# Performance work log

Measured on AMD Instinct MI355X. Metric: run time of the kernel, lower is better.

## Reference

```python
import jax, jax.numpy as jnp
import numpy as np

N = 10000       # n_nodes
E = 640000      # n_edges (avg degree 64)
D_IN = 128      # in_feats
D_H = 128       # n_hidden
N_CLS = 64      # n_classes


def setup_inputs() -> dict:
    key = jax.random.key(0)
    k1, k2, k3, k4, k5, k6 = jax.random.split(key, 6)
    features = jax.random.normal(k1, (N, D_IN), dtype=jnp.float32)
    src = jax.random.randint(k2, (E,), 0, N, dtype=jnp.int32)
    dst = jax.random.randint(k3, (E,), 0, N, dtype=jnp.int32)
    s = 0.05  # small init scale to keep activations bounded across 3 layers
    # Stored as [in, out]; equivalent to torch Linear weight [out, in] transposed.
    W0 = jax.random.normal(k4, (D_IN, D_H), dtype=jnp.float32) * s
    W1 = jax.random.normal(k5, (D_H, D_H), dtype=jnp.float32) * s
    W2 = jax.random.normal(k6, (D_H, N_CLS), dtype=jnp.float32) * s
    return {"features": features, "W0": W0, "W1": W1, "W2": W2,
            "src": src, "dst": dst}


def reference(features, W0, W1, W2, src, dst):
    # GINConv with aggregator 'sum', eps=0 (learn_eps=False):
    #   h' = Linear(h + sum_{(u->v) in E} h[u] scattered to v)
    # Dropout is identity at inference; 'activation' is unused in the module.
    def gin_layer(h, W):
        agg = jax.ops.segment_sum(h[src], dst, num_segments=N)  # [N, d]
        return (h + agg) @ W

    h = gin_layer(features, W0)
    h = gin_layer(h, W1)
    h = gin_layer(h, W2)
    return h
```

## Files before the change

kernel.cpp:

```cpp
#include <hip/hip_runtime.h>
#include <hip/hip_bf16.h>

#define NN 10000
#define NE 640000
#define D_IN 128
#define D_H 128
#define N_CLS 64
#define CAP 160
#define GRP 157
#define CAPC 4800
#define CCS 16
#define SENT 10000
#define EPB 1024
#define AB 625
#define CB 1251
#define WB 80

__device__ __forceinline__ float blo(unsigned u) { return __uint_as_float(u << 16); }
__device__ __forceinline__ float bhi(unsigned u) { return __uint_as_float(u & 0xffff0000u); }
__device__ __forceinline__ unsigned short f2bf(float f) {
    unsigned u = __float_as_uint(f);
    return (unsigned short)((u + 0x7fffu + ((u >> 16) & 1u)) >> 16);
}
__device__ __forceinline__ unsigned packbf(float a, float b) {
    return (unsigned)f2bf(a) | ((unsigned)f2bf(b) << 16);
}

__global__ __launch_bounds__(256) void prep_a(const int* __restrict__ src,
                                              const int* __restrict__ dst,
                                              int* __restrict__ coarse_cnt,
                                              unsigned* __restrict__ coarse,
                                              const float* __restrict__ feat,
                                              unsigned* __restrict__ hb0,
                                              const float* __restrict__ W0,
                                              const float* __restrict__ W1,
                                              const float* __restrict__ W2,
                                              unsigned* __restrict__ wb0,
                                              unsigned* __restrict__ wb1,
                                              unsigned* __restrict__ wb2) {
    int bid = blockIdx.x;
    if (bid >= AB + CB) {
        int t = (bid - AB - CB) * 256 + threadIdx.x;
        if (t < 8192) {
            int kp = t >> 7, j = t & 127;
            wb0[t] = packbf(W0[(2 * kp) * 128 + j], W0[(2 * kp + 1) * 128 + j]);
        } else if (t < 16384) {
            int tt = t - 8192, kp = tt >> 7, j = tt & 127;
            wb1[tt] = packbf(W1[(2 * kp) * 128 + j], W1[(2 * kp + 1) * 128 + j]);
        } else if (t < 20480) {
            int tt = t - 16384, kp = tt >> 6, j = tt & 63;
            wb2[tt] = packbf(W2[(2 * kp) * 64 + j], W2[(2 * kp + 1) * 64 + j]);
        }
        return;
    }
    if (bid >= AB) {
        int t = (bid - AB) * 256 + threadIdx.x;
        if (t < NN * 32) {
            float4 f = ((const float4*)feat)[t];
            ((uint2*)hb0)[t] = make_uint2(packbf(f.x, f.y), packbf(f.z, f.w));
        } else if (t < (NN + 1) * 32) {
            ((uint2*)hb0)[t] = make_uint2(0u, 0u);
        }
        return;
    }
    __shared__ unsigned stage[EPB];
    __shared__ int hist[GRP], gbase[GRP], cur[GRP];
    const int t = threadIdx.x;
    for (int i = t; i < GRP; i += 256) hist[i] = 0;
    __syncthreads();
    const int e0 = bid * EPB;
    for (int i = t; i < EPB; i += 256) {
        int s = src[e0 + i];
        int d = dst[e0 + i];
        stage[i] = (unsigned)s | ((unsigned)d << 16);
        atomicAdd(&hist[d >> 6], 1);
    }
    __syncthreads();
    for (int i = t; i < GRP; i += 256) {
        gbase[i] = atomicAdd(&coarse_cnt[i * CCS], hist[i]);
        cur[i] = 0;
    }
    __syncthreads();
    for (int i = t; i < EPB; i += 256) {
        unsigned u = stage[i];
        int g = u >> 22;
        int r = atomicAdd(&cur[g], 1);
        coarse[g * CAPC + gbase[g] + r] = u;
    }
}

__global__ __launch_bounds__(1024) void prep_b(const int* __restrict__ coarse_cnt,
                                               const unsigned* __restrict__ coarse,
                                               int* __restrict__ cnt,
                                               unsigned short* __restrict__ colbuf) {
    __shared__ int cur[64];
    __shared__ unsigned short sbuf[64][CAP];
    const int g = blockIdx.x;
    const int t = threadIdx.x;
    if (t < 64) cur[t] = 0;
    __syncthreads();
    const int m = coarse_cnt[g * CCS];
    const unsigned* cb = coarse + g * CAPC;
    for (int i = t; i < m; i += 1024) {
        unsigned u = cb[i];
        int s = (int)(u & 0xFFFFu);
        int dl = (int)(u >> 16) - (g << 6);
        int r = atomicAdd(&cur[dl], 1);
        sbuf[dl][r] = (unsigned short)s;
    }
    __syncthreads();
    if (t < 64) {
        int n = (g << 6) + t;
        if (n < NN) {
            int c = cur[t];
            int pad = (32 - (c & 31)) & 31;
            for (int k = 0; k < pad; ++k) sbuf[t][c + k] = (unsigned short)SENT;
            cnt[n] = c + pad;
        }
    }
    __syncthreads();
    const uint4* s4 = (const uint4*)sbuf;
    for (int idx = t; idx < 64 * (CAP / 8); idx += 1024) {
        int node = (g << 6) + (idx / (CAP / 8));
        if (node < NN)
            ((uint4*)colbuf)[(size_t)node * (CAP / 8) + (idx % (CAP / 8))] = s4[idx];
    }
}

__global__ __launch_bounds__(256, 4) void gin_layer1(const uint4* __restrict__ hb4,
                                                     const int* __restrict__ cnt,
                                                     const unsigned short* __restrict__ colbuf,
                                                     const unsigned* __restrict__ Wb,
                                                     unsigned short* __restrict__ outb) {
    constexpr int M = 4;
    __shared__ float xs[M][D_H];
    const int base = blockIdx.x * M;
    const int tid = threadIdx.x;
    const int wave = tid >> 6;
    const int lane = tid & 63;
    const int sub = lane >> 4;
    const int off = lane & 15;

    const int n = __builtin_amdgcn_readfirstlane(base + wave);
    float a0, a1, a2, a3, a4, a5, a6, a7;
    if (sub == 0) {
        uint4 u = hb4[n * 16 + off];
        a0 = blo(u.x); a1 = bhi(u.x); a2 = blo(u.y); a3 = bhi(u.y);
        a4 = blo(u.z); a5 = bhi(u.z); a6 = blo(u.w); a7 = bhi(u.w);
    } else {
        a0 = a1 = a2 = a3 = a4 = a5 = a6 = a7 = 0.f;
    }
    const int NCH = __builtin_amdgcn_readfirstlane(cnt[n]) >> 5;
    const uint2* cl = (const uint2*)(colbuf + n * CAP);
    const int sh = (sub & 1) << 4;
    uint2 p0 = cl[0], p1 = cl[1], p2 = cl[2], p3 = cl[3];
    uint2 p4 = cl[4], p5 = cl[5], p6 = cl[6], p7 = cl[7];
    for (int c = 0; c < NCH; ++c) {
        unsigned w0 = (sub & 2) ? p0.y : p0.x;
        unsigned w1 = (sub & 2) ? p1.y : p1.x;
        unsigned w2 = (sub & 2) ? p2.y : p2.x;
        unsigned w3 = (sub & 2) ? p3.y : p3.x;
        unsigned w4 = (sub & 2) ? p4.y : p4.x;
        unsigned w5 = (sub & 2) ? p5.y : p5.x;
        unsigned w6 = (sub & 2) ? p6.y : p6.x;
        unsigned w7 = (sub & 2) ? p7.y : p7.x;
        int s0 = (int)((w0 >> sh) & 0xffffu);
        int s1 = (int)((w1 >> sh) & 0xffffu);
        int s2 = (int)((w2 >> sh) & 0xffffu);
        int s3 = (int)((w3 >> sh) & 0xffffu);
        int s4 = (int)((w4 >> sh) & 0xffffu);
        int s5 = (int)((w5 >> sh) & 0xffffu);
        int s6 = (int)((w6 >> sh) & 0xffffu);
        int s7 = (int)((w7 >> sh) & 0xffffu);
        uint4 u0 = hb4[s0 * 16 + off];
        uint4 u1 = hb4[s1 * 16 + off];
        uint4 u2 = hb4[s2 * 16 + off];
        uint4 u3 = hb4[s3 * 16 + off];
        uint4 u4 = hb4[s4 * 16 + off];
        uint4 u5 = hb4[s5 * 16 + off];
        uint4 u6 = hb4[s6 * 16 + off];
        uint4 u7 = hb4[s7 * 16 + off];
        {
            const uint2* nx = cl + 8 * (c + 1);
            p0 = nx[0]; p1 = nx[1]; p2 = nx[2]; p3 = nx[3];
            p4 = nx[4]; p5 = nx[5]; p6 = nx[6]; p7 = nx[7];
        }
        a0 += ((blo(u0.x) + blo(u1.x)) + (blo(u2.x) + blo(u3.x)))
            + ((blo(u4.x) + blo(u5.x)) + (blo(u6.x) + blo(u7.x)));
        a1 += ((bhi(u0.x) + bhi(u1.x)) + (bhi(u2.x) + bhi(u3.x)))
            + ((bhi(u4.x) + bhi(u5.x)) + (bhi(u6.x) + bhi(u7.x)));
        a2 += ((blo(u0.y) + blo(u1.y)) + (blo(u2.y) + blo(u3.y)))
            + ((blo(u4.y) + blo(u5.y)) + (blo(u6.y) + blo(u7.y)));
        a3 += ((bhi(u0.y) + bhi(u1.y)) + (bhi(u2.y) + bhi(u3.y)))
            + ((bhi(u4.y) + bhi(u5.y)) + (bhi(u6.y) + bhi(u7.y)));
        a4 += ((blo(u0.z) + blo(u1.z)) + (blo(u2.z) + blo(u3.z)))
            + ((blo(u4.z) + blo(u5.z)) + (blo(u6.z) + blo(u7.z)));
        a5 += ((bhi(u0.z) + bhi(u1.z)) + (bhi(u2.z) + bhi(u3.z)))
            + ((bhi(u4.z) + bhi(u5.z)) + (bhi(u6.z) + bhi(u7.z)));
        a6 += ((blo(u0.w) + blo(u1.w)) + (blo(u2.w) + blo(u3.w)))
            + ((blo(u4.w) + blo(u5.w)) + (blo(u6.w) + blo(u7.w)));
        a7 += ((bhi(u0.w) + bhi(u1.w)) + (bhi(u2.w) + bhi(u3.w)))
            + ((bhi(u4.w) + bhi(u5.w)) + (bhi(u6.w) + bhi(u7.w)));
    }
    a0 += __shfl_xor(a0, 16); a0 += __shfl_xor(a0, 32);
    a1 += __shfl_xor(a1, 16); a1 += __shfl_xor(a1, 32);
    a2 += __shfl_xor(a2, 16); a2 += __shfl_xor(a2, 32);
    a3 += __shfl_xor(a3, 16); a3 += __shfl_xor(a3, 32);
    a4 += __shfl_xor(a4, 16); a4 += __shfl_xor(a4, 32);
    a5 += __shfl_xor(a5, 16); a5 += __shfl_xor(a5, 32);
    a6 += __shfl_xor(a6, 16); a6 += __shfl_xor(a6, 32);
    a7 += __shfl_xor(a7, 16); a7 += __shfl_xor(a7, 32);
    if (sub == 0) {
        *(float4*)&xs[wave][8 * off]     = make_float4(a0, a1, a2, a3);
        *(float4*)&xs[wave][8 * off + 4] = make_float4(a4, a5, a6, a7);
    }
    __syncthreads();

    constexpr int J = D_H;
    constexpr int G = 256 / J;
    constexpr int NM = M / G;
    const int gq = tid / J;
    const int j = tid % J;
    const int mbase = gq * NM;
    float acc[NM];
#pragma unroll
    for (int m = 0; m < NM; ++m) acc[m] = 0.f;
    for (int k = 0; k < D_H; k += 4) {
        unsigned wp0 = Wb[(k >> 1) * J + j];
        unsigned wp1 = Wb[((k >> 1) + 1) * J + j];
        float w0 = blo(wp0), w1 = bhi(wp0), w2 = blo(wp1), w3 = bhi(wp1);
#pragma unroll
        for (int m = 0; m < NM; ++m) {
            float4 xv = *(const float4*)&xs[mbase + m][k];
            acc[m] += xv.x * w0 + xv.y * w1 + xv.z * w2 + xv.w * w3;
        }
    }
#pragma unroll
    for (int m = 0; m < NM; ++m) {
        int n2 = base + mbase + m;
        outb[(size_t)n2 * J + j] = f2bf(acc[m]);
    }
    if (blockIdx.x == 0 && tid < 32) {
        ((uint2*)(outb + (size_t)SENT * D_H))[tid] = make_uint2(0u, 0u);
    }
}

__global__ __launch_bounds__(256, 4) void gin_mid(const uint4* __restrict__ hb4,
                                                  const int* __restrict__ cnt,
                                                  const unsigned short* __restrict__ colbuf,
                                                  const unsigned* __restrict__ Wb1,
                                                  const unsigned* __restrict__ Wb2,
                                                  unsigned short* __restrict__ tb) {
    constexpr int M = 4;
    __shared__ float xs[M][D_H];
    __shared__ float ys[M][136];
    const int base = blockIdx.x * M;
    const int tid = threadIdx.x;
    const int wave = tid >> 6;
    const int lane = tid & 63;
    const int sub = lane >> 4;
    const int off = lane & 15;

    const int n = __builtin_amdgcn_readfirstlane(base + wave);
    float a0, a1, a2, a3, a4, a5, a6, a7;
    if (sub == 0) {
        uint4 u = hb4[n * 16 + off];
        a0 = blo(u.x); a1 = bhi(u.x); a2 = blo(u.y); a3 = bhi(u.y);
        a4 = blo(u.z); a5 = bhi(u.z); a6 = blo(u.w); a7 = bhi(u.w);
    } else {
        a0 = a1 = a2 = a3 = a4 = a5 = a6 = a7 = 0.f;
    }
    const int NCH = __builtin_amdgcn_readfirstlane(cnt[n]) >> 5;
    const uint2* cl = (const uint2*)(colbuf + n * CAP);
    const int sh = (sub & 1) << 4;
    uint2 p0 = cl[0], p1 = cl[1], p2 = cl[2], p3 = cl[3];
    uint2 p4 = cl[4], p5 = cl[5], p6 = cl[6], p7 = cl[7];
    for (int c = 0; c < NCH; ++c) {
        unsigned w0 = (sub & 2) ? p0.y : p0.x;
        unsigned w1 = (sub & 2) ? p1.y : p1.x;
        unsigned w2 = (sub & 2) ? p2.y : p2.x;
        unsigned w3 = (sub & 2) ? p3.y : p3.x;
        unsigned w4 = (sub & 2) ? p4.y : p4.x;
        unsigned w5 = (sub & 2) ? p5.y : p5.x;
        unsigned w6 = (sub & 2) ? p6.y : p6.x;
        unsigned w7 = (sub & 2) ? p7.y : p7.x;
        int s0 = (int)((w0 >> sh) & 0xffffu);
        int s1 = (int)((w1 >> sh) & 0xffffu);
        int s2 = (int)((w2 >> sh) & 0xffffu);
        int s3 = (int)((w3 >> sh) & 0xffffu);
        int s4 = (int)((w4 >> sh) & 0xffffu);
        int s5 = (int)((w5 >> sh) & 0xffffu);
        int s6 = (int)((w6 >> sh) & 0xffffu);
        int s7 = (int)((w7 >> sh) & 0xffffu);
        uint4 u0 = hb4[s0 * 16 + off];
        uint4 u1 = hb4[s1 * 16 + off];
        uint4 u2 = hb4[s2 * 16 + off];
        uint4 u3 = hb4[s3 * 16 + off];
        uint4 u4 = hb4[s4 * 16 + off];
        uint4 u5 = hb4[s5 * 16 + off];
        uint4 u6 = hb4[s6 * 16 + off];
        uint4 u7 = hb4[s7 * 16 + off];
        {
            const uint2* nx = cl + 8 * (c + 1);
            p0 = nx[0]; p1 = nx[1]; p2 = nx[2]; p3 = nx[3];
            p4 = nx[4]; p5 = nx[5]; p6 = nx[6]; p7 = nx[7];
        }
        a0 += ((blo(u0.x) + blo(u1.x)) + (blo(u2.x) + blo(u3.x)))
            + ((blo(u4.x) + blo(u5.x)) + (blo(u6.x) + blo(u7.x)));
        a1 += ((bhi(u0.x) + bhi(u1.x)) + (bhi(u2.x) + bhi(u3.x)))
            + ((bhi(u4.x) + bhi(u5.x)) + (bhi(u6.x) + bhi(u7.x)));
        a2 += ((blo(u0.y) + blo(u1.y)) + (blo(u2.y) + blo(u3.y)))
            + ((blo(u4.y) + blo(u5.y)) + (blo(u6.y) + blo(u7.y)));
        a3 += ((bhi(u0.y) + bhi(u1.y)) + (bhi(u2.y) + bhi(u3.y)))
            + ((bhi(u4.y) + bhi(u5.y)) + (bhi(u6.y) + bhi(u7.y)));
        a4 += ((blo(u0.z) + blo(u1.z)) + (blo(u2.z) + blo(u3.z)))
            + ((blo(u4.z) + blo(u5.z)) + (blo(u6.z) + blo(u7.z)));
        a5 += ((bhi(u0.z) + bhi(u1.z)) + (bhi(u2.z) + bhi(u3.z)))
            + ((bhi(u4.z) + bhi(u5.z)) + (bhi(u6.z) + bhi(u7.z)));
        a6 += ((blo(u0.w) + blo(u1.w)) + (blo(u2.w) + blo(u3.w)))
            + ((blo(u4.w) + blo(u5.w)) + (blo(u6.w) + blo(u7.w)));
        a7 += ((bhi(u0.w) + bhi(u1.w)) + (bhi(u2.w) + bhi(u3.w)))
            + ((bhi(u4.w) + bhi(u5.w)) + (bhi(u6.w) + bhi(u7.w)));
    }
    a0 += __shfl_xor(a0, 16); a0 += __shfl_xor(a0, 32);
    a1 += __shfl_xor(a1, 16); a1 += __shfl_xor(a1, 32);
    a2 += __shfl_xor(a2, 16); a2 += __shfl_xor(a2, 32);
    a3 += __shfl_xor(a3, 16); a3 += __shfl_xor(a3, 32);
    a4 += __shfl_xor(a4, 16); a4 += __shfl_xor(a4, 32);
    a5 += __shfl_xor(a5, 16); a5 += __shfl_xor(a5, 32);
    a6 += __shfl_xor(a6, 16); a6 += __shfl_xor(a6, 32);
    a7 += __shfl_xor(a7, 16); a7 += __shfl_xor(a7, 32);
    if (sub == 0) {
        *(float4*)&xs[wave][8 * off]     = make_float4(a0, a1, a2, a3);
        *(float4*)&xs[wave][8 * off + 4] = make_float4(a4, a5, a6, a7);
    }
    __syncthreads();

    {
        constexpr int J = D_H;
        constexpr int G = 256 / J;
        constexpr int NM = M / G;
        const int gq = tid / J;
        const int j = tid % J;
        const int mbase = gq * NM;
        float acc[NM];
#pragma unroll
        for (int m = 0; m < NM; ++m) acc[m] = 0.f;
        for (int k = 0; k < D_H; k += 4) {
            unsigned wp0 = Wb1[(k >> 1) * J + j];
            unsigned wp1 = Wb1[((k >> 1) + 1) * J + j];
            float w0 = blo(wp0), w1 = bhi(wp0), w2 = blo(wp1), w3 = bhi(wp1);
#pragma unroll
            for (int m = 0; m < NM; ++m) {
                float4 xv = *(const float4*)&xs[mbase + m][k];
                acc[m] += xv.x * w0 + xv.y * w1 + xv.z * w2 + xv.w * w3;
            }
        }
#pragma unroll
        for (int m = 0; m < NM; ++m) ys[mbase + m][j] = acc[m];
    }
    __syncthreads();

    {
        constexpr int J = N_CLS;
        const int j = tid & 63;
        const int gm = tid >> 6;
        float acc = 0.f;
        for (int k = 0; k < D_H; k += 4) {
            unsigned wp0 = Wb2[(k >> 1) * J + j];
            unsigned wp1 = Wb2[((k >> 1) + 1) * J + j];
            float w0 = blo(wp0), w1 = bhi(wp0), w2 = blo(wp1), w3 = bhi(wp1);
            float4 xv = *(const float4*)&ys[gm][k];
            acc += xv.x * w0 + xv.y * w1 + xv.z * w2 + xv.w * w3;
        }
        tb[(size_t)(base + gm) * J + j] = f2bf(acc);
    }
    if (blockIdx.x == 0 && tid < 16) {
        ((uint2*)(tb + (size_t)SENT * N_CLS))[tid] = make_uint2(0u, 0u);
    }
}

__global__ __launch_bounds__(256, 4) void agg3(const uint4* __restrict__ tb4,
                                               const int* __restrict__ cnt,
                                               const unsigned short* __restrict__ colbuf,
                                               float* __restrict__ outf) {
    constexpr int M = 4;
    const int base = blockIdx.x * M;
    const int tid = threadIdx.x;
    const int wave = tid >> 6;
    const int lane = tid & 63;
    const int sub = lane >> 3;
    const int off = lane & 7;

    const int n = __builtin_amdgcn_readfirstlane(base + wave);
    float a0, a1, a2, a3, a4, a5, a6, a7;
    if (sub == 0) {
        uint4 u = tb4[n * 8 + off];
        a0 = blo(u.x); a1 = bhi(u.x); a2 = blo(u.y); a3 = bhi(u.y);
        a4 = blo(u.z); a5 = bhi(u.z); a6 = blo(u.w); a7 = bhi(u.w);
    } else {
        a0 = a1 = a2 = a3 = a4 = a5 = a6 = a7 = 0.f;
    }
    const int NCH = __builtin_amdgcn_readfirstlane(cnt[n]) >> 5;
    const uint2* cl = (const uint2*)(colbuf + n * CAP);
    const int hi4 = sub >> 2;
    const int wsel = (sub >> 1) & 1;
    const int sh = (sub & 1) << 4;
    uint2 p0 = cl[0], p1 = cl[1], p2 = cl[2], p3 = cl[3];
    uint2 p4 = cl[4], p5 = cl[5], p6 = cl[6], p7 = cl[7];
    for (int c = 0; c < NCH; ++c) {
        unsigned q0 = hi4 ? (wsel ? p1.y : p1.x) : (wsel ? p0.y : p0.x);
        unsigned q1 = hi4 ? (wsel ? p3.y : p3.x) : (wsel ? p2.y : p2.x);
        unsigned q2 = hi4 ? (wsel ? p5.y : p5.x) : (wsel ? p4.y : p4.x);
        unsigned q3 = hi4 ? (wsel ? p7.y : p7.x) : (wsel ? p6.y : p6.x);
        int s0 = (int)((q0 >> sh) & 0xffffu);
        int s1 = (int)((q1 >> sh) & 0xffffu);
        int s2 = (int)((q2 >> sh) & 0xffffu);
        int s3 = (int)((q3 >> sh) & 0xffffu);
        uint4 u0 = tb4[s0 * 8 + off];
        uint4 u1 = tb4[s1 * 8 + off];
        uint4 u2 = tb4[s2 * 8 + off];
        uint4 u3 = tb4[s3 * 8 + off];
        {
            const uint2* nx = cl + 8 * (c + 1);
            p0 = nx[0]; p1 = nx[1]; p2 = nx[2]; p3 = nx[3];
            p4 = nx[4]; p5 = nx[5]; p6 = nx[6]; p7 = nx[7];
        }
        a0 += (blo(u0.x) + blo(u1.x)) + (blo(u2.x) + blo(u3.x));
        a1 += (bhi(u0.x) + bhi(u1.x)) + (bhi(u2.x) + bhi(u3.x));
        a2 += (blo(u0.y) + blo(u1.y)) + (blo(u2.y) + blo(u3.y));
        a3 += (bhi(u0.y) + bhi(u1.y)) + (bhi(u2.y) + bhi(u3.y));
        a4 += (blo(u0.z) + blo(u1.z)) + (blo(u2.z) + blo(u3.z));
        a5 += (bhi(u0.z) + bhi(u1.z)) + (bhi(u2.z) + bhi(u3.z));
        a6 += (blo(u0.w) + blo(u1.w)) + (blo(u2.w) + blo(u3.w));
        a7 += (bhi(u0.w) + bhi(u1.w)) + (bhi(u2.w) + bhi(u3.w));
    }
    a0 += __shfl_xor(a0, 8); a0 += __shfl_xor(a0, 16); a0 += __shfl_xor(a0, 32);
    a1 += __shfl_xor(a1, 8); a1 += __shfl_xor(a1, 16); a1 += __shfl_xor(a1, 32);
    a2 += __shfl_xor(a2, 8); a2 += __shfl_xor(a2, 16); a2 += __shfl_xor(a2, 32);
    a3 += __shfl_xor(a3, 8); a3 += __shfl_xor(a3, 16); a3 += __shfl_xor(a3, 32);
    a4 += __shfl_xor(a4, 8); a4 += __shfl_xor(a4, 16); a4 += __shfl_xor(a4, 32);
    a5 += __shfl_xor(a5, 8); a5 += __shfl_xor(a5, 16); a5 += __shfl_xor(a5, 32);
    a6 += __shfl_xor(a6, 8); a6 += __shfl_xor(a6, 16); a6 += __shfl_xor(a6, 32);
    a7 += __shfl_xor(a7, 8); a7 += __shfl_xor(a7, 16); a7 += __shfl_xor(a7, 32);
    if (sub == 0) {
        float* o = outf + (size_t)n * N_CLS + 8 * off;
        *(float4*)o       = make_float4(a0, a1, a2, a3);
        *(float4*)(o + 4) = make_float4(a4, a5, a6, a7);
    }
}

extern "C" void kernel_launch(void* const* d_in, const int* in_sizes, int n_in,
                              void* d_out, int out_size, void* d_ws, size_t ws_size,
                              hipStream_t stream) {
    const float* feat = (const float*)d_in[0];
    const float* W0   = (const float*)d_in[1];
    const float* W1   = (const float*)d_in[2];
    const float* W2   = (const float*)d_in[3];
    const int*   src  = (const int*)d_in[4];
    const int*   dst  = (const int*)d_in[5];
    float* out = (float*)d_out;

    int* coarse_cnt        = (int*)d_ws;
    int* cnt               = coarse_cnt + GRP * CCS;
    unsigned short* colbuf = (unsigned short*)(cnt + NN + 8);
    unsigned* coarse       = (unsigned*)(colbuf + (size_t)NN * CAP);
    unsigned* hb0          = coarse + (size_t)GRP * CAPC;
    unsigned* hb1          = hb0 + (size_t)(NN + 1) * 64;
    unsigned* hb2          = hb1 + (size_t)(NN + 1) * 64;
    unsigned* wb0          = hb2 + (size_t)(NN + 1) * 64;
    unsigned* wb1          = wb0 + 8192;
    unsigned* wb2          = wb1 + 8192;
    unsigned short* tb     = (unsigned short*)hb2;

    hipMemsetAsync(coarse_cnt, 0, GRP * CCS * sizeof(int), stream);
    prep_a<<<AB + CB + WB, 256, 0, stream>>>(src, dst, coarse_cnt, coarse, feat, hb0,
                                             W0, W1, W2, wb0, wb1, wb2);
    prep_b<<<GRP, 1024, 0, stream>>>(coarse_cnt, coarse, cnt, colbuf);

    gin_layer1<<<NN / 4, 256, 0, stream>>>((const uint4*)hb0, cnt, colbuf, wb0,
                                           (unsigned short*)hb1);
    gin_mid<<<NN / 4, 256, 0, stream>>>((const uint4*)hb1, cnt, colbuf, wb1, wb2, tb);
    agg3<<<NN / 4, 256, 0, stream>>>((const uint4*)tb, cnt, colbuf, out);
}
```

Before: 142.9 us.

## Premultiply the three GIN weights and aggregate at 64-wide after one projection

Because the layers have no nonlinearity, the three weight matrices are multiplied together on device during prep (W0·W1, then ·W2, packed to bf16). The forward pass becomes one 128-wide aggregation with a single 128→64 projection, followed by two 64-wide aggregations. This removes the 128-wide middle gather and two per-node matmuls, cutting gather bandwidth. In exchange it adds small serial weight-product work in the prep kernels and changes bf16 rounding behaviour.

New measurement: 139.8 us. -2.2%, faster.

```diff
diff --git a/kernel.cpp b/kernel.cpp
--- a/kernel.cpp
+++ b/kernel.cpp
@@ -14,7 +14,8 @@
 #define EPB 1024
 #define AB 625
 #define CB 1251
-#define WB 80
+#define W01B 16
+#define WPB 4
 
 __device__ __forceinline__ float blo(unsigned u) { return __uint_as_float(u << 16); }
 __device__ __forceinline__ float bhi(unsigned u) { return __uint_as_float(u & 0xffff0000u); }
@@ -34,23 +35,19 @@
                                               unsigned* __restrict__ hb0,
                                               const float* __restrict__ W0,
                                               const float* __restrict__ W1,
-                                              const float* __restrict__ W2,
-                                              unsigned* __restrict__ wb0,
-                                              unsigned* __restrict__ wb1,
-                                              unsigned* __restrict__ wb2) {
+                                              float* __restrict__ W01) {
     int bid = blockIdx.x;
     if (bid >= AB + CB) {
         int t = (bid - AB - CB) * 256 + threadIdx.x;
-        if (t < 8192) {
-            int kp = t >> 7, j = t & 127;
-            wb0[t] = packbf(W0[(2 * kp) * 128 + j], W0[(2 * kp + 1) * 128 + j]);
-        } else if (t < 16384) {
-            int tt = t - 8192, kp = tt >> 7, j = tt & 127;
-            wb1[tt] = packbf(W1[(2 * kp) * 128 + j], W1[(2 * kp + 1) * 128 + j]);
-        } else if (t < 20480) {
-            int tt = t - 16384, kp = tt >> 6, j = tt & 63;
-            wb2[tt] = packbf(W2[(2 * kp) * 64 + j], W2[(2 * kp + 1) * 64 + j]);
-        }
+        int i = t >> 5;
+        int jb = (t & 31) << 2;
+        float c0 = 0.f, c1 = 0.f, c2 = 0.f, c3 = 0.f;
+        for (int k = 0; k < 128; ++k) {
+            float a = W0[i * 128 + k];
+            float4 b = *(const float4*)&W1[k * 128 + jb];
+            c0 += a * b.x; c1 += a * b.y; c2 += a * b.z; c3 += a * b.w;
+        }
+        *(float4*)&W01[i * 128 + jb] = make_float4(c0, c1, c2, c3);
         return;
     }
     if (bid >= AB) {
@@ -92,11 +89,28 @@
 __global__ __launch_bounds__(1024) void prep_b(const int* __restrict__ coarse_cnt,
                                                const unsigned* __restrict__ coarse,
                                                int* __restrict__ cnt,
-                                               unsigned short* __restrict__ colbuf) {
+                                               unsigned short* __restrict__ colbuf,
+                                               const float* __restrict__ W01,
+                                               const float* __restrict__ W2,
+                                               unsigned* __restrict__ wbp) {
+    const int g = blockIdx.x;
+    const int t = threadIdx.x;
+    if (g >= GRP) {
+        int s = (g - GRP) * 1024 + t;
+        int kp = s >> 6, j = s & 63;
+        float c0 = 0.f, c1 = 0.f;
+        const float* r0 = W01 + (2 * kp) * 128;
+        const float* r1 = r0 + 128;
+        for (int k = 0; k < 128; ++k) {
+            float w2 = W2[k * 64 + j];
+            c0 += r0[k] * w2;
+            c1 += r1[k] * w2;
+        }
+        wbp[kp * 64 + j] = packbf(c0, c1);
+        return;
+    }
     __shared__ int cur[64];
     __shared__ unsigned short sbuf[64][CAP];
-    const int g = blockIdx.x;
-    const int t = threadIdx.x;
     if (t < 64) cur[t] = 0;
     __syncthreads();
     const int m = coarse_cnt[g * CCS];
@@ -127,11 +141,11 @@
     }
 }
 
-__global__ __launch_bounds__(256, 4) void gin_layer1(const uint4* __restrict__ hb4,
-                                                     const int* __restrict__ cnt,
-                                                     const unsigned short* __restrict__ colbuf,
-                                                     const unsigned* __restrict__ Wb,
-                                                     unsigned short* __restrict__ outb) {
+__global__ __launch_bounds__(256, 4) void proj1(const uint4* __restrict__ hb4,
+                                                const int* __restrict__ cnt,
+                                                const unsigned short* __restrict__ colbuf,
+                                                const unsigned* __restrict__ Wbp,
+                                                unsigned short* __restrict__ tb) {
     constexpr int M = 4;
     __shared__ float xs[M][D_H];
     const int base = blockIdx.x * M;
@@ -216,174 +230,25 @@
     }
     __syncthreads();
 
-    constexpr int J = D_H;
-    constexpr int G = 256 / J;
-    constexpr int NM = M / G;
-    const int gq = tid / J;
-    const int j = tid % J;
-    const int mbase = gq * NM;
-    float acc[NM];
-#pragma unroll
-    for (int m = 0; m < NM; ++m) acc[m] = 0.f;
+    const int j = tid & 63;
+    float acc = 0.f;
     for (int k = 0; k < D_H; k += 4) {
-        unsigned wp0 = Wb[(k >> 1) * J + j];
-        unsigned wp1 = Wb[((k >> 1) + 1) * J + j];
+        unsigned wp0 = Wbp[(k >> 1) * 64 + j];
+        unsigned wp1 = Wbp[((k >> 1) + 1) * 64 + j];
         float w0 = blo(wp0), w1 = bhi(wp0), w2 = blo(wp1), w3 = bhi(wp1);
-#pragma unroll
-        for (int m = 0; m < NM; ++m) {
-            float4 xv = *(const float4*)&xs[mbase + m][k];
-            acc[m] += xv.x * w0 + xv.y * w1 + xv.z * w2 + xv.w * w3;
-        }
-    }
-#pragma unroll
-    for (int m = 0; m < NM; ++m) {
-        int n2 = base + mbase + m;
-        outb[(size_t)n2 * J + j] = f2bf(acc[m]);
-    }
-    if (blockIdx.x == 0 && tid < 32) {
-        ((uint2*)(outb + (size_t)SENT * D_H))[tid] = make_uint2(0u, 0u);
-    }
-}
-
-__global__ __launch_bounds__(256, 4) void gin_mid(const uint4* __restrict__ hb4,
-                                                  const int* __restrict__ cnt,
-                                                  const unsigned short* __restrict__ colbuf,
-                                                  const unsigned* __restrict__ Wb1,
-                                                  const unsigned* __restrict__ Wb2,
-                                                  unsigned short* __restrict__ tb) {
-    constexpr int M = 4;
-    __shared__ float xs[M][D_H];
-    __shared__ float ys[M][136];
-    const int base = blockIdx.x * M;
-    const int tid = threadIdx.x;
-    const int wave = tid >> 6;
-    const int lane = tid & 63;
-    const int sub = lane >> 4;
-    const int off = lane & 15;
-
-    const int n = __builtin_amdgcn_readfirstlane(base + wave);
-    float a0, a1, a2, a3, a4, a5, a6, a7;
-    if (sub == 0) {
-        uint4 u = hb4[n * 16 + off];
-        a0 = blo(u.x); a1 = bhi(u.x); a2 = blo(u.y); a3 = bhi(u.y);
-        a4 = blo(u.z); a5 = bhi(u.z); a6 = blo(u.w); a7 = bhi(u.w);
-    } else {
-        a0 = a1 = a2 = a3 = a4 = a5 = a6 = a7 = 0.f;
-    }
-    const int NCH = __builtin_amdgcn_readfirstlane(cnt[n]) >> 5;
-    const uint2* cl = (const uint2*)(colbuf + n * CAP);
-    const int sh = (sub & 1) << 4;
-    uint2 p0 = cl[0], p1 = cl[1], p2 = cl[2], p3 = cl[3];
-    uint2 p4 = cl[4], p5 = cl[5], p6 = cl[6], p7 = cl[7];
-    for (int c = 0; c < NCH; ++c) {
-        unsigned w0 = (sub & 2) ? p0.y : p0.x;
-        unsigned w1 = (sub & 2) ? p1.y : p1.x;
-        unsigned w2 = (sub & 2) ? p2.y : p2.x;
-        unsigned w3 = (sub & 2) ? p3.y : p3.x;
-        unsigned w4 = (sub & 2) ? p4.y : p4.x;
-        unsigned w5 = (sub & 2) ? p5.y : p5.x;
-        unsigned w6 = (sub & 2) ? p6.y : p6.x;
-        unsigned w7 = (sub & 2) ? p7.y : p7.x;
-        int s0 = (int)((w0 >> sh) & 0xffffu);
-        int s1 = (int)((w1 >> sh) & 0xffffu);
-        int s2 = (int)((w2 >> sh) & 0xffffu);
-        int s3 = (int)((w3 >> sh) & 0xffffu);
-        int s4 = (int)((w4 >> sh) & 0xffffu);
-        int s5 = (int)((w5 >> sh) & 0xffffu);
-        int s6 = (int)((w6 >> sh) & 0xffffu);
-        int s7 = (int)((w7 >> sh) & 0xffffu);
-        uint4 u0 = hb4[s0 * 16 + off];
-        uint4 u1 = hb4[s1 * 16 + off];
-        uint4 u2 = hb4[s2 * 16 + off];
-        uint4 u3 = hb4[s3 * 16 + off];
-        uint4 u4 = hb4[s4 * 16 + off];
-        uint4 u5 = hb4[s5 * 16 + off];
-        uint4 u6 = hb4[s6 * 16 + off];
-        uint4 u7 = hb4[s7 * 16 + off];
-        {
-            const uint2* nx = cl + 8 * (c + 1);
-            p0 = nx[0]; p1 = nx[1]; p2 = nx[2]; p3 = nx[3];
-            p4 = nx[4]; p5 = nx[5]; p6 = nx[6]; p7 = nx[7];
-        }
-        a0 += ((blo(u0.x) + blo(u1.x)) + (blo(u2.x) + blo(u3.x)))
-            + ((blo(u4.x) + blo(u5.x)) + (blo(u6.x) + blo(u7.x)));
-        a1 += ((bhi(u0.x) + bhi(u1.x)) + (bhi(u2.x) + bhi(u3.x)))
-            + ((bhi(u4.x) + bhi(u5.x)) + (bhi(u6.x) + bhi(u7.x)));
-        a2 += ((blo(u0.y) + blo(u1.y)) + (blo(u2.y) + blo(u3.y)))
-            + ((blo(u4.y) + blo(u5.y)) + (blo(u6.y) + blo(u7.y)));
-        a3 += ((bhi(u0.y) + bhi(u1.y)) + (bhi(u2.y) + bhi(u3.y)))
-            + ((bhi(u4.y) + bhi(u5.y)) + (bhi(u6.y) + bhi(u7.y)));
-        a4 += ((blo(u0.z) + blo(u1.z)) + (blo(u2.z) + blo(u3.z)))
-            + ((blo(u4.z) + blo(u5.z)) + (blo(u6.z) + blo(u7.z)));
-        a5 += ((bhi(u0.z) + bhi(u1.z)) + (bhi(u2.z) + bhi(u3.z)))
-            + ((bhi(u4.z) + bhi(u5.z)) + (bhi(u6.z) + bhi(u7.z)));
-        a6 += ((blo(u0.w) + blo(u1.w)) + (blo(u2.w) + blo(u3.w)))
-            + ((blo(u4.w) + blo(u5.w)) + (blo(u6.w) + blo(u7.w)));
-        a7 += ((bhi(u0.w) + bhi(u1.w)) + (bhi(u2.w) + bhi(u3.w)))
-            + ((bhi(u4.w) + bhi(u5.w)) + (bhi(u6.w) + bhi(u7.w)));
-    }
-    a0 += __shfl_xor(a0, 16); a0 += __shfl_xor(a0, 32);
-    a1 += __shfl_xor(a1, 16); a1 += __shfl_xor(a1, 32);
-    a2 += __shfl_xor(a2, 16); a2 += __shfl_xor(a2, 32);
-    a3 += __shfl_xor(a3, 16); a3 += __shfl_xor(a3, 32);
-    a4 += __shfl_xor(a4, 16); a4 += __shfl_xor(a4, 32);
-    a5 += __shfl_xor(a5, 16); a5 += __shfl_xor(a5, 32);
-    a6 += __shfl_xor(a6, 16); a6 += __shfl_xor(a6, 32);
-    a7 += __shfl_xor(a7, 16); a7 += __shfl_xor(a7, 32);
-    if (sub == 0) {
-        *(float4*)&xs[wave][8 * off]     = make_float4(a0, a1, a2, a3);
-        *(float4*)&xs[wave][8 * off + 4] = make_float4(a4, a5, a6, a7);
-    }
-    __syncthreads();
-
-    {
-        constexpr int J = D_H;
-        constexpr int G = 256 / J;
-        constexpr int NM = M / G;
-        const int gq = tid / J;
-        const int j = tid % J;
-        const int mbase = gq * NM;
-        float acc[NM];
-#pragma unroll
-        for (int m = 0; m < NM; ++m) acc[m] = 0.f;
-        for (int k = 0; k < D_H; k += 4) {
-            unsigned wp0 = Wb1[(k >> 1) * J + j];
-            unsigned wp1 = Wb1[((k >> 1) + 1) * J + j];
-            float w0 = blo(wp0), w1 = bhi(wp0), w2 = blo(wp1), w3 = bhi(wp1);
-#pragma unroll
-            for (int m = 0; m < NM; ++m) {
-                float4 xv = *(const float4*)&xs[mbase + m][k];
-                acc[m] += xv.x * w0 + xv.y * w1 + xv.z * w2 + xv.w * w3;
-            }
-        }
-#pragma unroll
-        for (int m = 0; m < NM; ++m) ys[mbase + m][j] = acc[m];
-    }
-    __syncthreads();
-
-    {
-        constexpr int J = N_CLS;
-        const int j = tid & 63;
-        const int gm = tid >> 6;
-        float acc = 0.f;
-        for (int k = 0; k < D_H; k += 4) {
-            unsigned wp0 = Wb2[(k >> 1) * J + j];
-            unsigned wp1 = Wb2[((k >> 1) + 1) * J + j];
-            float w0 = blo(wp0), w1 = bhi(wp0), w2 = blo(wp1), w3 = bhi(wp1);
-            float4 xv = *(const float4*)&ys[gm][k];
-            acc += xv.x * w0 + xv.y * w1 + xv.z * w2 + xv.w * w3;
-        }
-        tb[(size_t)(base + gm) * J + j] = f2bf(acc);
-    }
+        float4 xv = *(const float4*)&xs[wave][k];
+        acc += xv.x * w0 + xv.y * w1 + xv.z * w2 + xv.w * w3;
+    }
+    tb[(size_t)(base + wave) * 64 + j] = f2bf(acc);
     if (blockIdx.x == 0 && tid < 16) {
-        ((uint2*)(tb + (size_t)SENT * N_CLS))[tid] = make_uint2(0u, 0u);
-    }
-}
-
-__global__ __launch_bounds__(256, 4) void agg3(const uint4* __restrict__ tb4,
-                                               const int* __restrict__ cnt,
-                                               const unsigned short* __restrict__ colbuf,
-                                               float* __restrict__ outf) {
+        ((uint2*)(tb + (size_t)SENT * 64))[tid] = make_uint2(0u, 0u);
+    }
+}
+
+__global__ __launch_bounds__(256, 4) void agg64b(const uint4* __restrict__ tb4,
+                                                 const int* __restrict__ cnt,
+                                                 const unsigned short* __restrict__ colbuf,
+                                                 unsigned short* __restrict__ tb2) {
     constexpr int M = 4;
     const int base = blockIdx.x * M;
     const int tid = threadIdx.x;
@@ -444,6 +309,79 @@
     a6 += __shfl_xor(a6, 8); a6 += __shfl_xor(a6, 16); a6 += __shfl_xor(a6, 32);
     a7 += __shfl_xor(a7, 8); a7 += __shfl_xor(a7, 16); a7 += __shfl_xor(a7, 32);
     if (sub == 0) {
+        unsigned short* o = tb2 + (size_t)n * 64 + 8 * off;
+        *(uint4*)o = make_uint4(packbf(a0, a1), packbf(a2, a3),
+                                packbf(a4, a5), packbf(a6, a7));
+    }
+    if (blockIdx.x == 0 && tid < 16) {
+        ((uint2*)(tb2 + (size_t)SENT * 64))[tid] = make_uint2(0u, 0u);
+    }
+}
+
+__global__ __launch_bounds__(256, 4) void agg64f(const uint4* __restrict__ tb4,
+                                                 const int* __restrict__ cnt,
+                                                 const unsigned short* __restrict__ colbuf,
+                                                 float* __restrict__ outf) {
+    constexpr int M = 4;
+    const int base = blockIdx.x * M;
+    const int tid = threadIdx.x;
+    const int wave = tid >> 6;
+    const int lane = tid & 63;
+    const int sub = lane >> 3;
+    const int off = lane & 7;
+
+    const int n = __builtin_amdgcn_readfirstlane(base + wave);
+    float a0, a1, a2, a3, a4, a5, a6, a7;
+    if (sub == 0) {
+        uint4 u = tb4[n * 8 + off];
+        a0 = blo(u.x); a1 = bhi(u.x); a2 = blo(u.y); a3 = bhi(u.y);
+        a4 = blo(u.z); a5 = bhi(u.z); a6 = blo(u.w); a7 = bhi(u.w);
+    } else {
+        a0 = a1 = a2 = a3 = a4 = a5 = a6 = a7 = 0.f;
+    }
+    const int NCH = __builtin_amdgcn_readfirstlane(cnt[n]) >> 5;
+    const uint2* cl = (const uint2*)(colbuf + n * CAP);
+    const int hi4 = sub >> 2;
+    const int wsel = (sub >> 1) & 1;
+    const int sh = (sub & 1) << 4;
+    uint2 p0 = cl[0], p1 = cl[1], p2 = cl[2], p3 = cl[3];
+    uint2 p4 = cl[4], p5 = cl[5], p6 = cl[6], p7 = cl[7];
+    for (int c = 0; c < NCH; ++c) {
+        unsigned q0 = hi4 ? (wsel ? p1.y : p1.x) : (wsel ? p0.y : p0.x);
+        unsigned q1 = hi4 ? (wsel ? p3.y : p3.x) : (wsel ? p2.y : p2.x);
+        unsigned q2 = hi4 ? (wsel ? p5.y : p5.x) : (wsel ? p4.y : p4.x);
+        unsigned q3 = hi4 ? (wsel ? p7.y : p7.x) : (wsel ? p6.y : p6.x);
+        int s0 = (int)((q0 >> sh) & 0xffffu);
+        int s1 = (int)((q1 >> sh) & 0xffffu);
+        int s2 = (int)((q2 >> sh) & 0xffffu);
+        int s3 = (int)((q3 >> sh) & 0xffffu);
+        uint4 u0 = tb4[s0 * 8 + off];
+        uint4 u1 = tb4[s1 * 8 + off];
+        uint4 u2 = tb4[s2 * 8 + off];
+        uint4 u3 = tb4[s3 * 8 + off];
+        {
+            const uint2* nx = cl + 8 * (c + 1);
+            p0 = nx[0]; p1 = nx[1]; p2 = nx[2]; p3 = nx[3];
+            p4 = nx[4]; p5 = nx[5]; p6 = nx[6]; p7 = nx[7];
+        }
+        a0 += (blo(u0.x) + blo(u1.x)) + (blo(u2.x) + blo(u3.x));
+        a1 += (bhi(u0.x) + bhi(u1.x)) + (bhi(u2.x) + bhi(u3.x));
+        a2 += (blo(u0.y) + blo(u1.y)) + (blo(u2.y) + blo(u3.y));
+        a3 += (bhi(u0.y) + bhi(u1.y)) + (bhi(u2.y) + bhi(u3.y));
+        a4 += (blo(u0.z) + blo(u1.z)) + (blo(u2.z) + blo(u3.z));
+        a5 += (bhi(u0.z) + bhi(u1.z)) + (bhi(u2.z) + bhi(u3.z));
+        a6 += (blo(u0.w) + blo(u1.w)) + (blo(u2.w) + blo(u3.w));
+        a7 += (bhi(u0.w) + bhi(u1.w)) + (bhi(u2.w) + bhi(u3.w));
+    }
+    a0 += __shfl_xor(a0, 8); a0 += __shfl_xor(a0, 16); a0 += __shfl_xor(a0, 32);
+    a1 += __shfl_xor(a1, 8); a1 += __shfl_xor(a1, 16); a1 += __shfl_xor(a1, 32);
+    a2 += __shfl_xor(a2, 8); a2 += __shfl_xor(a2, 16); a2 += __shfl_xor(a2, 32);
+    a3 += __shfl_xor(a3, 8); a3 += __shfl_xor(a3, 16); a3 += __shfl_xor(a3, 32);
+    a4 += __shfl_xor(a4, 8); a4 += __shfl_xor(a4, 16); a4 += __shfl_xor(a4, 32);
+    a5 += __shfl_xor(a5, 8); a5 += __shfl_xor(a5, 16); a5 += __shfl_xor(a5, 32);
+    a6 += __shfl_xor(a6, 8); a6 += __shfl_xor(a6, 16); a6 += __shfl_xor(a6, 32);
+    a7 += __shfl_xor(a7, 8); a7 += __shfl_xor(a7, 16); a7 += __shfl_xor(a7, 32);
+    if (sub == 0) {
         float* o = outf + (size_t)n * N_CLS + 8 * off;
         *(float4*)o       = make_float4(a0, a1, a2, a3);
         *(float4*)(o + 4) = make_float4(a4, a5, a6, a7);
@@ -466,20 +404,20 @@
     unsigned short* colbuf = (unsigned short*)(cnt + NN + 8);
     unsigned* coarse       = (unsigned*)(colbuf + (size_t)NN * CAP);
     unsigned* hb0          = coarse + (size_t)GRP * CAPC;
-    unsigned* hb1          = hb0 + (size_t)(NN + 1) * 64;
-    unsigned* hb2          = hb1 + (size_t)(NN + 1) * 64;
-    unsigned* wb0          = hb2 + (size_t)(NN + 1) * 64;
-    unsigned* wb1          = wb0 + 8192;
-    unsigned* wb2          = wb1 + 8192;
-    unsigned short* tb     = (unsigned short*)hb2;
+    unsigned* tbu          = hb0 + (size_t)(NN + 1) * 64;
+    unsigned* tb2u         = tbu + (size_t)(NN + 1) * 32;
+    float* W01             = (float*)(tb2u + (size_t)(NN + 1) * 32);
+    unsigned* wbp          = (unsigned*)(W01 + 16384);
+    unsigned short* tb     = (unsigned short*)tbu;
+    unsigned short* tb2    = (unsigned short*)tb2u;
 
     hipMemsetAsync(coarse_cnt, 0, GRP * CCS * sizeof(int), stream);
-    prep_a<<<AB + CB + WB, 256, 0, stream>>>(src, dst, coarse_cnt, coarse, feat, hb0,
-                                             W0, W1, W2, wb0, wb1, wb2);
-    prep_b<<<GRP, 1024, 0, stream>>>(coarse_cnt, coarse, cnt, colbuf);
-
-    gin_layer1<<<NN / 4, 256, 0, stream>>>((const uint4*)hb0, cnt, colbuf, wb0,
-                                           (unsigned short*)hb1);
-    gin_mid<<<NN / 4, 256, 0, stream>>>((const uint4*)hb1, cnt, colbuf, wb1, wb2, tb);
-    agg3<<<NN / 4, 256, 0, stream>>>((const uint4*)tb, cnt, colbuf, out);
-}
+    prep_a<<<AB + CB + W01B, 256, 0, stream>>>(src, dst, coarse_cnt, coarse, feat, hb0,
+                                               W0, W1, W01);
+    prep_b<<<GRP + WPB, 1024, 0, stream>>>(coarse_cnt, coarse, cnt, colbuf,
+                                           W01, W2, wbp);
+
+    proj1<<<NN / 4, 256, 0, stream>>>((const uint4*)hb0, cnt, colbuf, wbp, tb);
+    agg64b<<<NN / 4, 256, 0, stream>>>((const uint4*)tb, cnt, colbuf, tb2);
+    agg64f<<<NN / 4, 256, 0, stream>>>((const uint4*)tb2, cnt, colbuf, out);
+}
```
